# Optimization experiments

Measured on AMD Instinct MI355X. Metric: run time of the kernel, lower is better.

## Reference

```python
import jax, jax.numpy as jnp
import numpy as np

A, B, O, ACT, H, NH = 16, 8192, 128, 16, 128, 4
D = H // NH  # attend_dim
IN = O + ACT
NEG = -1e9


def setup_inputs() -> dict:
    key = jax.random.key(0)
    ks = jax.random.split(key, 16)
    s = lambda k, shape, fan: jax.random.normal(k, shape, jnp.float32) / np.sqrt(fan)
    return {
        "obs": jax.random.normal(ks[0], (A, B, O), jnp.float32),
        "actions": jax.random.uniform(ks[1], (A, B, ACT), jnp.float32),
        # per-agent sa-encoder (enc_fc1)
        "W_sa": s(ks[2], (A, IN, H), IN), "b_sa": jnp.zeros((A, H), jnp.float32),
        # per-agent state encoder (s_enc_fc1)
        "W_s": s(ks[3], (A, O, H), O), "b_s": jnp.zeros((A, H), jnp.float32),
        # shared per-head extractors
        "Wk": s(ks[4], (NH, H, D), H),
        "Wsel": s(ks[5], (NH, H, D), H),
        "Wv": s(ks[6], (NH, H, D), H), "bv": jnp.zeros((NH, D), jnp.float32),
        # per-agent critic MLP
        "Wc1": s(ks[7], (A, 2 * H, H), 2 * H), "bc1": jnp.zeros((A, H), jnp.float32),
        "Wc2": s(ks[8], (A, H, ACT), H), "bc2": jnp.zeros((A, ACT), jnp.float32),
    }


def _bn(x):
    # BatchNorm1d(affine=False) in training mode: normalize over batch axis, biased var
    m = x.mean(axis=1, keepdims=True)
    v = x.var(axis=1, keepdims=True)
    return (x - m) / jnp.sqrt(v + 1e-5)


def reference(obs, actions, W_sa, b_sa, W_s, b_s, Wk, Wsel, Wv, bv, Wc1, bc1, Wc2, bc2):
    lrelu = jax.nn.leaky_relu  # slope 0.01, matches torch default
    inp = jnp.concatenate([obs, actions], axis=-1)            # [A,B,IN]
    sa = lrelu(jnp.einsum('abi,aih->abh', _bn(inp), W_sa) + b_sa[:, None, :])  # [A,B,H]
    se = lrelu(jnp.einsum('abo,aoh->abh', _bn(obs), W_s) + b_s[:, None, :])    # [A,B,H]
    keys = jnp.einsum('abh,nhd->nabd', sa, Wk)                # [NH,A,B,D]
    vals = lrelu(jnp.einsum('abh,nhd->nabd', sa, Wv) + bv[:, None, None, :])
    sel = jnp.einsum('abh,nhd->nabd', se, Wsel)
    logits = jnp.einsum('nibd,njbd->nibj', sel, keys) / np.sqrt(D)  # [NH,A,B,A]
    self_mask = jnp.eye(A, dtype=bool)[None, :, None, :]      # mask j == i
    w = jax.nn.softmax(jnp.where(self_mask, NEG, logits), axis=-1)
    other = jnp.einsum('nibj,njbd->nibd', w, vals)            # [NH,A,B,D]
    other = jnp.transpose(other, (1, 2, 0, 3)).reshape(A, B, NH * D)  # head-order concat
    cin = jnp.concatenate([se, other], axis=-1)               # [A,B,2H]
    h = lrelu(jnp.einsum('abk,akh->abh', cin, Wc1) + bc1[:, None, :])
    all_q = jnp.einsum('abh,aho->abo', h, Wc2) + bc2[:, None, :]      # [A,B,ACT]
    idx = jnp.argmax(actions, axis=-1)[..., None]             # int_acs, [A,B,1]
    q = jnp.take_along_axis(all_q, idx, axis=-1)              # [A,B,1]
    return q
```

## Files before the change

### kernel.cpp

```cpp
#include <hip/hip_runtime.h>
#include <hip/hip_bf16.h>

#define A_N 16
#define B_N 8192
#define O_N 128
#define ACT_N 16
#define H_N 128
#define NH_N 4
#define D_N 32
#define IN_N 144
#define NEGV -1e9f

typedef __attribute__((ext_vector_type(8))) short short8;
typedef __attribute__((ext_vector_type(4))) float floatx4;

static __device__ inline unsigned short f2bf(float f) {
    union { float f; unsigned u; } x{f};
    unsigned u = x.u + 0x7FFFu + ((x.u >> 16) & 1u);
    return (unsigned short)(u >> 16);
}
static __device__ inline unsigned pack_bf2(float a, float b) {
    union { float f; unsigned u; } xa{a}, xb{b};
    unsigned ua = xa.u + 0x7FFFu + ((xa.u >> 16) & 1u);
    unsigned ub = xb.u + 0x7FFFu + ((xb.u >> 16) & 1u);
    return (ua >> 16) | (ub & 0xFFFF0000u);
}
static __device__ inline float bf2f(unsigned short h) {
    union { unsigned u; float f; } x;
    x.u = ((unsigned)h) << 16;
    return x.f;
}
static __device__ inline float bflo(unsigned u) {
    union { unsigned u; float f; } x; x.u = u << 16; return x.f;
}
static __device__ inline float bfhi(unsigned u) {
    union { unsigned u; float f; } x; x.u = u & 0xFFFF0000u; return x.f;
}
static __device__ inline short8 ld_frag(const unsigned* p) {
    union { unsigned u[4]; short8 v; } x;
    uint2 lo = *(const uint2*)p;
    uint2 hi = *(const uint2*)(p + 2);
    x.u[0] = lo.x; x.u[1] = lo.y; x.u[2] = hi.x; x.u[3] = hi.y;
    return x.v;
}

__global__ __launch_bounds__(256) void k_zero(float* p, int n) {
    int i = blockIdx.x * 256 + threadIdx.x;
    if (i < n) p[i] = 0.f;
}

__global__ __launch_bounds__(256) void k_stats(const float* __restrict__ obs,
                                               const float* __restrict__ act,
                                               float* __restrict__ gsum,
                                               float* __restrict__ gsq) {
    __shared__ float ssum[IN_N];
    __shared__ float ssq[IN_N];
    int a = blockIdx.x >> 5;
    int r0 = (blockIdx.x & 31) * 256;
    int t = threadIdx.x;
    if (t < IN_N) { ssum[t] = 0.f; ssq[t] = 0.f; }
    __syncthreads();
    if (t < 128) {
        const float* p = obs + ((size_t)a * B_N + r0) * O_N + t;
        float s = 0.f, q = 0.f;
#pragma unroll 4
        for (int r = 0; r < 256; ++r) {
            float v = p[(size_t)r * O_N];
            s += v; q += v * v;
        }
        ssum[t] = s; ssq[t] = q;
    } else {
        int tt = t - 128;
        int f = tt & 15, rg = tt >> 4;
        const float* p = act + ((size_t)a * B_N + r0 + rg) * ACT_N + f;
        float s = 0.f, q = 0.f;
#pragma unroll 4
        for (int i = 0; i < 32; ++i) {
            float v = p[(size_t)i * 8 * ACT_N];
            s += v; q += v * v;
        }
        atomicAdd(&ssum[O_N + f], s);
        atomicAdd(&ssq[O_N + f], q);
    }
    __syncthreads();
    if (t < IN_N) {
        atomicAdd(&gsum[a * IN_N + t], ssum[t]);
        atomicAdd(&gsq[a * IN_N + t], ssq[t]);
    }
}

__global__ __launch_bounds__(256) void k_finalize(float* gsum, float* gsq) {
    int i = blockIdx.x * 256 + threadIdx.x;
    if (i < A_N * IN_N) {
        const float invB = 1.f / (float)B_N;
        float m = gsum[i] * invB;
        float v = fmaxf(gsq[i] * invB - m * m, 0.f);
        gsum[i] = m;
        gsq[i] = rsqrtf(v + 1e-5f);
    }
}

#define L1E 393216
#define P1E 409600
#define P2E 417792
#define CRE 679936
#define C2E 712704
__global__ __launch_bounds__(256) void k_wprep(
    const float* __restrict__ W_sa, const float* __restrict__ W_s,
    const float* __restrict__ Wk, const float* __restrict__ Wsel,
    const float* __restrict__ Wv, const float* __restrict__ Wc1,
    const float* __restrict__ Wc2, const float* __restrict__ rstd,
    unsigned* __restrict__ wt_l1, unsigned* __restrict__ wt_p1,
    unsigned* __restrict__ wt_p2, unsigned* __restrict__ wt_cr,
    float* __restrict__ wt_c2) {
    int idx = blockIdx.x * 256 + threadIdx.x;
    if (idx < L1E) {
        int a = idx / 24576, rem = idx % 24576;
        int n = rem & 255, kp = rem >> 8;
        int k0 = 2 * kp, k1 = k0 + 1;
        float v0 = 0.f, v1 = 0.f;
        if (n < 128) {
            if (k0 < IN_N) v0 = W_sa[((size_t)a * IN_N + k0) * H_N + n] * rstd[a * IN_N + k0];
            if (k1 < IN_N) v1 = W_sa[((size_t)a * IN_N + k1) * H_N + n] * rstd[a * IN_N + k1];
        } else {
            int m = n - 128;
            if (k0 < O_N) v0 = W_s[((size_t)a * O_N + k0) * H_N + m] * rstd[a * IN_N + k0];
            if (k1 < O_N) v1 = W_s[((size_t)a * O_N + k1) * H_N + m] * rstd[a * IN_N + k1];
        }
        wt_l1[(size_t)a * 24576 + n * 96 + kp] = pack_bf2(v0, v1);
    } else if (idx < P1E) {
        int i2 = idx - L1E;
        int n = i2 & 255, kp = i2 >> 8;
        int k0 = 2 * kp;
        float v0, v1;
        if (n < 128) {
            const float* w = Wk + ((size_t)(n >> 5) * H_N) * D_N + (n & 31);
            v0 = w[(size_t)k0 * D_N]; v1 = w[(size_t)(k0 + 1) * D_N];
        } else {
            int m = n - 128;
            const float* w = Wv + ((size_t)(m >> 5) * H_N) * D_N + (m & 31);
            v0 = w[(size_t)k0 * D_N]; v1 = w[(size_t)(k0 + 1) * D_N];
        }
        wt_p1[n * 64 + kp] = pack_bf2(v0, v1);
    } else if (idx < P2E) {
        int i3 = idx - P1E;
        int n = i3 & 127, kp = i3 >> 7;
        int k0 = 2 * kp;
        const float* w = Wsel + ((size_t)(n >> 5) * H_N) * D_N + (n & 31);
        wt_p2[n * 64 + kp] = pack_bf2(w[(size_t)k0 * D_N], w[(size_t)(k0 + 1) * D_N]);
    } else if (idx < CRE) {
        int i4 = idx - P2E;
        int a = i4 >> 14, r = i4 & 16383;
        int n = r & 127, kp = r >> 7;
        int k0 = 2 * kp;
        const float* w = Wc1 + (size_t)a * 256 * H_N + n;
        wt_cr[(size_t)a * 16384 + n * 128 + kp] =
            pack_bf2(w[(size_t)k0 * H_N], w[(size_t)(k0 + 1) * H_N]);
    } else if (idx < C2E) {
        int i5 = idx - CRE;
        int a = i5 >> 11, rem = i5 & 2047;
        int oo = rem >> 7, h = rem & 127;
        wt_c2[i5] = Wc2[((size_t)a * H_N + h) * ACT_N + oo];
    }
}

__global__ __launch_bounds__(256) void k_bfold(
    const float* __restrict__ mean, const float* __restrict__ rstd,
    const float* __restrict__ W_sa, const float* __restrict__ W_s,
    const float* __restrict__ b_sa, const float* __restrict__ b_s,
    float* __restrict__ fb) {
    int a = blockIdx.x, c = threadIdx.x;
    float s = 0.f;
    if (c < 128) {
        for (int k = 0; k < IN_N; ++k)
            s += mean[a * IN_N + k] * rstd[a * IN_N + k] *
                 W_sa[((size_t)a * IN_N + k) * H_N + c];
        fb[a * 128 + c] = b_sa[a * H_N + c] - s;
    } else {
        int m = c - 128;
        for (int k = 0; k < O_N; ++k)
            s += mean[a * IN_N + k] * rstd[a * IN_N + k] *
                 W_s[((size_t)a * O_N + k) * H_N + m];
        fb[2048 + a * 128 + m] = b_s[a * H_N + m] - s;
    }
}

__global__ __launch_bounds__(256, 3) void k_l1(
    const float* __restrict__ obs, const float* __restrict__ act,
    const unsigned* __restrict__ wt_l1, const float* __restrict__ fb,
    unsigned short* __restrict__ sa_us, unsigned short* __restrict__ se_us,
    int b0g, int Bc) {
    __shared__ unsigned smem[(128 + 128) * 34];
    unsigned* Xs = smem;
    unsigned* Ws = smem + 128 * 34;

    int a = blockIdx.y;
    int z = blockIdx.z;
    int b0 = blockIdx.x * 128;
    int t = threadIdx.x;
    int wid = t >> 6, lane = t & 63, lm = lane & 15, lq = lane >> 4;
    int wrow = (wid & 1) * 64;
    int wcol = (wid >> 1) * 64;

    int kchunks = z ? 2 : 3;
    int kstop = z ? 128 : 160;
    const float* bias = fb + z * 2048 + a * 128;
    unsigned short* outp = z ? se_us : sa_us;

    floatx4 acc[4][4];
#pragma unroll
    for (int mt = 0; mt < 4; ++mt)
#pragma unroll
        for (int nt = 0; nt < 4; ++nt)
#pragma unroll
            for (int e = 0; e < 4; ++e) acc[mt][nt][e] = 0.f;

    const unsigned* WtA = wt_l1 + (size_t)a * 24576 + (size_t)(z * 128) * 96;

    for (int c = 0; c < kchunks; ++c) {
        int kk = c * 64;
        __syncthreads();
        for (int idx = t; idx < 128 * 16; idx += 256) {
            int r = idx >> 4, c4 = idx & 15;
            int k = kk + c4 * 4;
            size_t grow = (size_t)a * B_N + b0g + b0 + r;
            float4 v;
            if (k < O_N) v = *(const float4*)&obs[grow * O_N + k];
            else if (!z && k < IN_N) v = *(const float4*)&act[grow * ACT_N + (k - O_N)];
            else v = make_float4(0.f, 0.f, 0.f, 0.f);
            uint2* dst = (uint2*)&Xs[r * 34 + c4 * 2];
            *dst = make_uint2(pack_bf2(v.x, v.y), pack_bf2(v.z, v.w));
        }
        for (int idx = t; idx < 128 * 8; idx += 256) {
            int n = idx >> 3, c4 = idx & 7;
            uint4 w = *(const uint4*)&WtA[(size_t)n * 96 + (kk >> 1) + c4 * 4];
            uint2* dst = (uint2*)&Ws[n * 34 + c4 * 4];
            dst[0] = make_uint2(w.x, w.y);
            dst[1] = make_uint2(w.z, w.w);
        }
        __syncthreads();
#pragma unroll
        for (int s = 0; s < 2; ++s) {
            if (kk + s * 32 >= kstop) break;
            short8 afr[4];
#pragma unroll
            for (int mt = 0; mt < 4; ++mt)
                afr[mt] = ld_frag(&Xs[(wrow + mt * 16 + lm) * 34 + s * 16 + lq * 4]);
#pragma unroll
            for (int nt = 0; nt < 4; ++nt) {
                short8 bfr = ld_frag(&Ws[(wcol + nt * 16 + lm) * 34 + s * 16 + lq * 4]);
#pragma unroll
                for (int mt = 0; mt < 4; ++mt)
                    acc[mt][nt] = __builtin_amdgcn_mfma_f32_16x16x32_bf16(
                        afr[mt], bfr, acc[mt][nt], 0, 0, 0);
            }
        }
    }

#pragma unroll
    for (int mt = 0; mt < 4; ++mt)
#pragma unroll
        for (int nt = 0; nt < 4; ++nt)
#pragma unroll
            for (int r = 0; r < 4; ++r) {
                int row = b0 + wrow + mt * 16 + lq * 4 + r;
                int col = wcol + nt * 16 + lm;
                float v = acc[mt][nt][r] + bias[col];
                v = v > 0.f ? v : 0.01f * v;
                outp[((size_t)a * Bc + row) * 128 + col] = f2bf(v);
            }
}

__global__ __launch_bounds__(256, 3) void k_fused(
    const unsigned* __restrict__ sa_u, const unsigned* __restrict__ se_u,
    const unsigned* __restrict__ wt_p1, const unsigned* __restrict__ wt_p2,
    const float* __restrict__ bv, unsigned short* __restrict__ other_us,
    int Bc) {
    __shared__ unsigned Xs[64 * 66];
    __shared__ unsigned short keys_s[64 * 130];
    __shared__ unsigned short vals_s[64 * 136];
    unsigned short* sel_s = (unsigned short*)Xs;

    int bg0 = blockIdx.x * 4;
    int t = threadIdx.x;
    int wid = t >> 6, lane = t & 63, lm = lane & 15, lq = lane >> 4;
    int wcol = wid * 32;

    for (int idx = t; idx < 64 * 16; idx += 256) {
        int r = idx >> 4, c4 = idx & 15;
        int a = r >> 2, b = bg0 + (r & 3);
        uint4 v = *(const uint4*)&sa_u[((size_t)a * Bc + b) * 64 + c4 * 4];
        uint2* dst = (uint2*)&Xs[r * 66 + c4 * 4];
        dst[0] = make_uint2(v.x, v.y);
        dst[1] = make_uint2(v.z, v.w);
    }
    uint4 seR[4];
#pragma unroll
    for (int ii = 0; ii < 4; ++ii) {
        int idx = t + ii * 256;
        int r = idx >> 4, c4 = idx & 15;
        int a = r >> 2, b = bg0 + (r & 3);
        seR[ii] = *(const uint4*)&se_u[((size_t)a * Bc + b) * 64 + c4 * 4];
    }
    __syncthreads();

#pragma unroll
    for (int pass = 0; pass < 2; ++pass) {
        floatx4 acc[4][2];
#pragma unroll
        for (int mt = 0; mt < 4; ++mt)
#pragma unroll
            for (int nt = 0; nt < 2; ++nt)
#pragma unroll
                for (int e = 0; e < 4; ++e) acc[mt][nt][e] = 0.f;
        const unsigned* wbase = wt_p1 + (size_t)(pass * 128) * 64;
#pragma unroll
        for (int s = 0; s < 4; ++s) {
            short8 afr[4];
#pragma unroll
            for (int mt = 0; mt < 4; ++mt)
                afr[mt] = ld_frag(&Xs[(mt * 16 + lm) * 66 + s * 16 + lq * 4]);
#pragma unroll
            for (int nt = 0; nt < 2; ++nt) {
                int col = wcol + nt * 16 + lm;
                short8 bfr = ld_frag(wbase + (size_t)col * 64 + s * 16 + lq * 4);
#pragma unroll
                for (int mt = 0; mt < 4; ++mt)
                    acc[mt][nt] = __builtin_amdgcn_mfma_f32_16x16x32_bf16(
                        afr[mt], bfr, acc[mt][nt], 0, 0, 0);
            }
        }
#pragma unroll
        for (int mt = 0; mt < 4; ++mt)
#pragma unroll
            for (int nt = 0; nt < 2; ++nt)
#pragma unroll
                for (int r = 0; r < 4; ++r) {
                    int row = mt * 16 + lq * 4 + r;
                    int col = wcol + nt * 16 + lm;
                    float v = acc[mt][nt][r];
                    if (pass == 0) {
                        keys_s[row * 130 + col] = f2bf(v);
                    } else {
                        v += bv[col];
                        v = v > 0.f ? v : 0.01f * v;
                        vals_s[row * 136 + col] = f2bf(v);
                    }
                }
    }
    __syncthreads();

#pragma unroll
    for (int ii = 0; ii < 4; ++ii) {
        int idx = t + ii * 256;
        int r = idx >> 4, c4 = idx & 15;
        uint2* dst = (uint2*)&Xs[r * 66 + c4 * 4];
        dst[0] = make_uint2(seR[ii].x, seR[ii].y);
        dst[1] = make_uint2(seR[ii].z, seR[ii].w);
    }
    __syncthreads();

    {
        floatx4 acc[4][2];
#pragma unroll
        for (int mt = 0; mt < 4; ++mt)
#pragma unroll
            for (int nt = 0; nt < 2; ++nt)
#pragma unroll
                for (int e = 0; e < 4; ++e) acc[mt][nt][e] = 0.f;
#pragma unroll
        for (int s = 0; s < 4; ++s) {
            short8 afr[4];
#pragma unroll
            for (int mt = 0; mt < 4; ++mt)
                afr[mt] = ld_frag(&Xs[(mt * 16 + lm) * 66 + s * 16 + lq * 4]);
#pragma unroll
            for (int nt = 0; nt < 2; ++nt) {
                int col = wcol + nt * 16 + lm;
                short8 bfr = ld_frag(wt_p2 + (size_t)col * 64 + s * 16 + lq * 4);
#pragma unroll
                for (int mt = 0; mt < 4; ++mt)
                    acc[mt][nt] = __builtin_amdgcn_mfma_f32_16x16x32_bf16(
                        afr[mt], bfr, acc[mt][nt], 0, 0, 0);
            }
        }
        __syncthreads();
#pragma unroll
        for (int mt = 0; mt < 4; ++mt)
#pragma unroll
            for (int nt = 0; nt < 2; ++nt)
#pragma unroll
                for (int r = 0; r < 4; ++r) {
                    int row = mt * 16 + lq * 4 + r;
                    int col = wcol + nt * 16 + lm;
                    sel_s[row * 130 + col] = f2bf(acc[mt][nt][r]);
                }
    }
    __syncthreads();

    const unsigned* keysU = (const unsigned*)keys_s;
    floatx4 lgacc[4];
#pragma unroll
    for (int n = 0; n < 4; ++n) {
        short8 afr = ld_frag(&Xs[(lm * 4 + wid) * 65 + n * 16 + lq * 4]);
        short8 bfr = ld_frag(&keysU[(lm * 4 + wid) * 65 + n * 16 + lq * 4]);
        floatx4 z4 = {0.f, 0.f, 0.f, 0.f};
        lgacc[n] = __builtin_amdgcn_mfma_f32_16x16x32_bf16(afr, bfr, z4, 0, 0, 0);
    }
    __syncthreads();

    float* lgs = (float*)keys_s;
#pragma unroll
    for (int n = 0; n < 4; ++n)
#pragma unroll
        for (int r = 0; r < 4; ++r) {
            int i = lq * 4 + r;
            lgs[((wid * 4 + n) * 16 + i) * 16 + lm] =
                lgacc[n][r] * 0.17677669529663687f;
        }

    int bsub = wid, n = (t >> 4) & 3, i = t & 15;
    float lg[16];
    {
        const float4* lgp = (const float4*)&lgs[((bsub * 4 + n) * 16 + i) * 16];
#pragma unroll
        for (int c = 0; c < 4; ++c) {
            float4 v = lgp[c];
            lg[4 * c] = v.x; lg[4 * c + 1] = v.y;
            lg[4 * c + 2] = v.z; lg[4 * c + 3] = v.w;
        }
    }
    lg[i] = NEGV;
    float m = lg[0];
#pragma unroll
    for (int j = 1; j < 16; ++j) m = fmaxf(m, lg[j]);
    float sum = 0.f;
#pragma unroll
    for (int j = 0; j < 16; ++j) { lg[j] = __expf(lg[j] - m); sum += lg[j]; }
    float inv = 1.f / sum;
#pragma unroll
    for (int j = 0; j < 16; ++j) lg[j] *= inv;

    const unsigned* valsU = (const unsigned*)vals_s;
    float ov[32];
#pragma unroll
    for (int u = 0; u < 32; ++u) ov[u] = 0.f;
#pragma unroll
    for (int j = 0; j < 16; ++j) {
        const uint4* vrow = (const uint4*)&valsU[(j * 4 + bsub) * 68 + n * 16];
        float w = lg[j];
#pragma unroll
        for (int c = 0; c < 4; ++c) {
            uint4 x = vrow[c];
            ov[8 * c + 0] = fmaf(w, bflo(x.x), ov[8 * c + 0]);
            ov[8 * c + 1] = fmaf(w, bfhi(x.x), ov[8 * c + 1]);
            ov[8 * c + 2] = fmaf(w, bflo(x.y), ov[8 * c + 2]);
            ov[8 * c + 3] = fmaf(w, bfhi(x.y), ov[8 * c + 3]);
            ov[8 * c + 4] = fmaf(w, bflo(x.z), ov[8 * c + 4]);
            ov[8 * c + 5] = fmaf(w, bfhi(x.z), ov[8 * c + 5]);
            ov[8 * c + 6] = fmaf(w, bflo(x.w), ov[8 * c + 6]);
            ov[8 * c + 7] = fmaf(w, bfhi(x.w), ov[8 * c + 7]);
        }
    }
    {
        uint4* orow = (uint4*)&other_us[((size_t)i * Bc + bg0 + bsub) * 128 + n * 32];
#pragma unroll
        for (int h = 0; h < 2; ++h) {
            uint4 o;
            o.x = pack_bf2(ov[16 * h + 0], ov[16 * h + 1]);
            o.y = pack_bf2(ov[16 * h + 2], ov[16 * h + 3]);
            o.z = pack_bf2(ov[16 * h + 4], ov[16 * h + 5]);
            o.w = pack_bf2(ov[16 * h + 6], ov[16 * h + 7]);
            orow[2 * h] = o;
            o.x = pack_bf2(ov[16 * h + 8], ov[16 * h + 9]);
            o.y = pack_bf2(ov[16 * h + 10], ov[16 * h + 11]);
            o.z = pack_bf2(ov[16 * h + 12], ov[16 * h + 13]);
            o.w = pack_bf2(ov[16 * h + 14], ov[16 * h + 15]);
            orow[2 * h + 1] = o;
        }
    }
}

__global__ __launch_bounds__(256, 3) void k_critic(
    const unsigned* __restrict__ se_u, const unsigned* __restrict__ other_u,
    const unsigned* __restrict__ wt_cr,
    const float* __restrict__ bc1, const float* __restrict__ actions,
    const float* __restrict__ wt_c2, const float* __restrict__ bc2,
    float* __restrict__ qout, int b0g, int Bc) {
    __shared__ unsigned smem[(64 + 128) * 34];
    unsigned* Xs = smem;
    unsigned* Ws = smem + 64 * 34;

    int a = blockIdx.y;
    int b0 = blockIdx.x * 64;
    int t = threadIdx.x;
    int wid = t >> 6, lane = t & 63, lm = lane & 15, lq = lane >> 4;
    int wrow = (wid & 1) * 32;
    int wcol = (wid >> 1) * 64;

    floatx4 acc[2][4];
#pragma unroll
    for (int mt = 0; mt < 2; ++mt)
#pragma unroll
        for (int nt = 0; nt < 4; ++nt)
#pragma unroll
            for (int e = 0; e < 4; ++e) acc[mt][nt][e] = 0.f;

    const unsigned* WtA = wt_cr + (size_t)a * 16384;

    for (int c = 0; c < 4; ++c) {
        int kk = c * 64;
        __syncthreads();
        const unsigned* src = (c < 2) ? se_u : other_u;
        int off = (c & 1) * 32;
        for (int idx = t; idx < 64 * 8; idx += 256) {
            int r = idx >> 3, c4 = idx & 7;
            uint4 v = *(const uint4*)&src[((size_t)a * Bc + b0 + r) * 64 + off + c4 * 4];
            uint2* dst = (uint2*)&Xs[r * 34 + c4 * 4];
            dst[0] = make_uint2(v.x, v.y);
            dst[1] = make_uint2(v.z, v.w);
        }
        for (int idx = t; idx < 128 * 8; idx += 256) {
            int n = idx >> 3, c4 = idx & 7;
            uint4 w = *(const uint4*)&WtA[(size_t)n * 128 + (kk >> 1) + c4 * 4];
            uint2* dst = (uint2*)&Ws[n * 34 + c4 * 4];
            dst[0] = make_uint2(w.x, w.y);
            dst[1] = make_uint2(w.z, w.w);
        }
        __syncthreads();
#pragma unroll
        for (int s = 0; s < 2; ++s) {
            short8 afr[2];
#pragma unroll
            for (int mt = 0; mt < 2; ++mt)
                afr[mt] = ld_frag(&Xs[(wrow + mt * 16 + lm) * 34 + s * 16 + lq * 4]);
#pragma unroll
            for (int nt = 0; nt < 4; ++nt) {
                short8 bfr = ld_frag(&Ws[(wcol + nt * 16 + lm) * 34 + s * 16 + lq * 4]);
#pragma unroll
                for (int mt = 0; mt < 2; ++mt)
                    acc[mt][nt] = __builtin_amdgcn_mfma_f32_16x16x32_bf16(
                        afr[mt], bfr, acc[mt][nt], 0, 0, 0);
            }
        }
    }

    __syncthreads();
    unsigned short* hbuf = (unsigned short*)smem;
#pragma unroll
    for (int mt = 0; mt < 2; ++mt)
#pragma unroll
        for (int nt = 0; nt < 4; ++nt)
#pragma unroll
            for (int r = 0; r < 4; ++r) {
                int row = wrow + mt * 16 + lq * 4 + r;
                int col = wcol + nt * 16 + lm;
                float v = acc[mt][nt][r] + bc1[a * H_N + col];
                v = v > 0.f ? v : 0.01f * v;
                hbuf[row * 132 + col] = f2bf(v);
            }
    __syncthreads();
    if (t < 64) {
        size_t arow = (size_t)a * B_N + b0g + b0 + t;
        const float* ap = &actions[arow * ACT_N];
        float bestv = ap[0];
        int bi = 0;
        for (int o = 1; o < ACT_N; ++o) {
            float v = ap[o];
            if (v > bestv) { bestv = v; bi = o; }
        }
        float q = bc2[a * ACT_N + bi];
        const float4* w4p = (const float4*)&wt_c2[((size_t)a * ACT_N + bi) * H_N];
        const uint2* hp2 = (const uint2*)&hbuf[t * 132];
#pragma unroll
        for (int h4 = 0; h4 < 32; ++h4) {
            float4 w4 = w4p[h4];
            uint2 hh = hp2[h4];
            q = fmaf(bflo(hh.x), w4.x, q);
            q = fmaf(bfhi(hh.x), w4.y, q);
            q = fmaf(bflo(hh.y), w4.z, q);
            q = fmaf(bfhi(hh.y), w4.w, q);
        }
        qout[arow] = q;
    }
}

extern "C" void kernel_launch(void* const* d_in, const int* in_sizes, int n_in,
                              void* d_out, int out_size, void* d_ws, size_t ws_size,
                              hipStream_t stream) {
    const float* obs     = (const float*)d_in[0];
    const float* actions = (const float*)d_in[1];
    const float* W_sa    = (const float*)d_in[2];
    const float* b_sa    = (const float*)d_in[3];
    const float* W_s     = (const float*)d_in[4];
    const float* b_s     = (const float*)d_in[5];
    const float* Wk      = (const float*)d_in[6];
    const float* Wsel    = (const float*)d_in[7];
    const float* Wv      = (const float*)d_in[8];
    const float* bv      = (const float*)d_in[9];
    const float* Wc1     = (const float*)d_in[10];
    const float* bc1     = (const float*)d_in[11];
    const float* Wc2     = (const float*)d_in[12];
    const float* bc2     = (const float*)d_in[13];
    float* out = (float*)d_out;
    char* ws = (char*)d_ws;

    size_t o = 0;
    float* gsum = (float*)(ws + o); o += 2304 * 4;
    float* gsq  = (float*)(ws + o); o += 2304 * 4;
    unsigned* wt_l1 = (unsigned*)(ws + o); o += (size_t)393216 * 4;
    unsigned* wt_p1 = (unsigned*)(ws + o); o += (size_t)16384 * 4;
    unsigned* wt_p2 = (unsigned*)(ws + o); o += (size_t)8192 * 4;
    unsigned* wt_cr = (unsigned*)(ws + o); o += (size_t)262144 * 4;
    float* fb = (float*)(ws + o); o += (size_t)4096 * 4;
    float* wt_c2 = (float*)(ws + o); o += (size_t)32768 * 4;
    size_t fixed = o;

    int Bc = B_N;
    while (Bc > 128 && fixed + 12288ull * Bc > ws_size) Bc >>= 1;

    unsigned short* sa_us = (unsigned short*)(ws + o); o += (size_t)A_N * Bc * 128 * 2;
    unsigned short* se_us = (unsigned short*)(ws + o); o += (size_t)A_N * Bc * 128 * 2;
    unsigned short* ot_us = (unsigned short*)(ws + o); o += (size_t)A_N * Bc * 128 * 2;

    k_zero<<<dim3(18), 256, 0, stream>>>(gsum, 2 * A_N * IN_N);
    k_stats<<<dim3(A_N * 32), 256, 0, stream>>>(obs, actions, gsum, gsq);
    k_finalize<<<dim3(9), 256, 0, stream>>>(gsum, gsq);
    k_wprep<<<dim3(C2E / 256), 256, 0, stream>>>(W_sa, W_s, Wk, Wsel, Wv, Wc1, Wc2,
                                                 gsq, wt_l1, wt_p1, wt_p2, wt_cr, wt_c2);
    k_bfold<<<dim3(A_N), 256, 0, stream>>>(gsum, gsq, W_sa, W_s, b_sa, b_s, fb);

    for (int b0g = 0; b0g < B_N; b0g += Bc) {
        k_l1<<<dim3(Bc / 128, A_N, 2), 256, 0, stream>>>(
            obs, actions, wt_l1, fb, sa_us, se_us, b0g, Bc);
        k_fused<<<dim3(Bc / 4), 256, 0, stream>>>(
            (const unsigned*)sa_us, (const unsigned*)se_us, wt_p1, wt_p2, bv,
            ot_us, Bc);
        k_critic<<<dim3(Bc / 64, A_N), 256, 0, stream>>>(
            (const unsigned*)se_us, (const unsigned*)ot_us, wt_cr, bc1,
            actions, wt_c2, bc2, out, b0g, Bc);
    }
}
```

Before: 324.9 us.

## Merge sa/se encoder blocks and switch intermediates to batch-major agent-interleaved layout

k_l1 now computes both the sa and se encoders in one 512-thread block, so each obs tile is loaded and converted to bf16 once instead of twice. The sa/se/other intermediates are stored as [B][A][H] instead of [A][B][H], which makes k_fused's per-batch-group gather a contiguous read and changes k_critic to a strided per-agent read. LDS strides and row orderings in k_fused are adjusted to match the new layout, and k_critic's occupancy hint is raised. The se half of the merged block still runs the padded actions chunk through the zero-weight rows, and the critic reads are less coalesced.

```diff
diff --git a/kernel.cpp b/kernel.cpp
--- a/kernel.cpp
+++ b/kernel.cpp
@@ -185,28 +185,22 @@
     }
 }
 
-__global__ __launch_bounds__(256, 3) void k_l1(
+__global__ __launch_bounds__(512, 2) void k_l1(
     const float* __restrict__ obs, const float* __restrict__ act,
     const unsigned* __restrict__ wt_l1, const float* __restrict__ fb,
     unsigned short* __restrict__ sa_us, unsigned short* __restrict__ se_us,
     int b0g, int Bc) {
-    __shared__ unsigned smem[(128 + 128) * 34];
+    __shared__ unsigned smem[(128 + 256) * 34];
     unsigned* Xs = smem;
     unsigned* Ws = smem + 128 * 34;
 
     int a = blockIdx.y;
-    int z = blockIdx.z;
     int b0 = blockIdx.x * 128;
     int t = threadIdx.x;
     int wid = t >> 6, lane = t & 63, lm = lane & 15, lq = lane >> 4;
     int wrow = (wid & 1) * 64;
     int wcol = (wid >> 1) * 64;
 
-    int kchunks = z ? 2 : 3;
-    int kstop = z ? 128 : 160;
-    const float* bias = fb + z * 2048 + a * 128;
-    unsigned short* outp = z ? se_us : sa_us;
-
     floatx4 acc[4][4];
 #pragma unroll
     for (int mt = 0; mt < 4; ++mt)
@@ -215,23 +209,23 @@
 #pragma unroll
             for (int e = 0; e < 4; ++e) acc[mt][nt][e] = 0.f;
 
-    const unsigned* WtA = wt_l1 + (size_t)a * 24576 + (size_t)(z * 128) * 96;
-
-    for (int c = 0; c < kchunks; ++c) {
+    const unsigned* WtA = wt_l1 + (size_t)a * 24576;
+
+    for (int c = 0; c < 3; ++c) {
         int kk = c * 64;
         __syncthreads();
-        for (int idx = t; idx < 128 * 16; idx += 256) {
+        for (int idx = t; idx < 128 * 16; idx += 512) {
             int r = idx >> 4, c4 = idx & 15;
             int k = kk + c4 * 4;
             size_t grow = (size_t)a * B_N + b0g + b0 + r;
             float4 v;
             if (k < O_N) v = *(const float4*)&obs[grow * O_N + k];
-            else if (!z && k < IN_N) v = *(const float4*)&act[grow * ACT_N + (k - O_N)];
+            else if (k < IN_N) v = *(const float4*)&act[grow * ACT_N + (k - O_N)];
             else v = make_float4(0.f, 0.f, 0.f, 0.f);
             uint2* dst = (uint2*)&Xs[r * 34 + c4 * 2];
             *dst = make_uint2(pack_bf2(v.x, v.y), pack_bf2(v.z, v.w));
         }
-        for (int idx = t; idx < 128 * 8; idx += 256) {
+        for (int idx = t; idx < 256 * 8; idx += 512) {
             int n = idx >> 3, c4 = idx & 7;
             uint4 w = *(const uint4*)&WtA[(size_t)n * 96 + (kk >> 1) + c4 * 4];
             uint2* dst = (uint2*)&Ws[n * 34 + c4 * 4];
@@ -241,7 +235,7 @@
         __syncthreads();
 #pragma unroll
         for (int s = 0; s < 2; ++s) {
-            if (kk + s * 32 >= kstop) break;
+            if (kk + s * 32 >= 160) break;
             short8 afr[4];
 #pragma unroll
             for (int mt = 0; mt < 4; ++mt)
@@ -257,17 +251,21 @@
         }
     }
 
+    int zsel = (wcol >= 128);
+    unsigned short* outp = zsel ? se_us : sa_us;
+    const float* bias = fb + zsel * 2048 + a * 128;
+    int cbase = wcol & 127;
 #pragma unroll
     for (int mt = 0; mt < 4; ++mt)
 #pragma unroll
         for (int nt = 0; nt < 4; ++nt)
 #pragma unroll
             for (int r = 0; r < 4; ++r) {
-                int row = b0 + wrow + mt * 16 + lq * 4 + r;
-                int col = wcol + nt * 16 + lm;
+                int row = wrow + mt * 16 + lq * 4 + r;
+                int col = cbase + nt * 16 + lm;
                 float v = acc[mt][nt][r] + bias[col];
                 v = v > 0.f ? v : 0.01f * v;
-                outp[((size_t)a * Bc + row) * 128 + col] = f2bf(v);
+                outp[((size_t)(b0 + row) * 16 + a) * 128 + col] = f2bf(v);
             }
 }
 
@@ -286,10 +284,12 @@
     int wid = t >> 6, lane = t & 63, lm = lane & 15, lq = lane >> 4;
     int wcol = wid * 32;
 
+    const unsigned* sa_base = sa_u + (size_t)(bg0 * 16) * 64;
+    const unsigned* se_base = se_u + (size_t)(bg0 * 16) * 64;
+
     for (int idx = t; idx < 64 * 16; idx += 256) {
         int r = idx >> 4, c4 = idx & 15;
-        int a = r >> 2, b = bg0 + (r & 3);
-        uint4 v = *(const uint4*)&sa_u[((size_t)a * Bc + b) * 64 + c4 * 4];
+        uint4 v = *(const uint4*)&sa_base[(size_t)idx * 4];
         uint2* dst = (uint2*)&Xs[r * 66 + c4 * 4];
         dst[0] = make_uint2(v.x, v.y);
         dst[1] = make_uint2(v.z, v.w);
@@ -298,9 +298,7 @@
 #pragma unroll
     for (int ii = 0; ii < 4; ++ii) {
         int idx = t + ii * 256;
-        int r = idx >> 4, c4 = idx & 15;
-        int a = r >> 2, b = bg0 + (r & 3);
-        seR[ii] = *(const uint4*)&se_u[((size_t)a * Bc + b) * 64 + c4 * 4];
+        seR[ii] = *(const uint4*)&se_base[(size_t)idx * 4];
     }
     __syncthreads();
 
@@ -393,7 +391,7 @@
                 for (int r = 0; r < 4; ++r) {
                     int row = mt * 16 + lq * 4 + r;
                     int col = wcol + nt * 16 + lm;
-                    sel_s[row * 130 + col] = f2bf(acc[mt][nt][r]);
+                    sel_s[row * 132 + col] = f2bf(acc[mt][nt][r]);
                 }
     }
     __syncthreads();
@@ -402,8 +400,8 @@
     floatx4 lgacc[4];
 #pragma unroll
     for (int n = 0; n < 4; ++n) {
-        short8 afr = ld_frag(&Xs[(lm * 4 + wid) * 65 + n * 16 + lq * 4]);
-        short8 bfr = ld_frag(&keysU[(lm * 4 + wid) * 65 + n * 16 + lq * 4]);
+        short8 afr = ld_frag(&Xs[(wid * 16 + lm) * 66 + n * 16 + lq * 4]);
+        short8 bfr = ld_frag(&keysU[(wid * 16 + lm) * 65 + n * 16 + lq * 4]);
         floatx4 z4 = {0.f, 0.f, 0.f, 0.f};
         lgacc[n] = __builtin_amdgcn_mfma_f32_16x16x32_bf16(afr, bfr, z4, 0, 0, 0);
     }
@@ -447,7 +445,7 @@
     for (int u = 0; u < 32; ++u) ov[u] = 0.f;
 #pragma unroll
     for (int j = 0; j < 16; ++j) {
-        const uint4* vrow = (const uint4*)&valsU[(j * 4 + bsub) * 68 + n * 16];
+        const uint4* vrow = (const uint4*)&valsU[(bsub * 16 + j) * 68 + n * 16];
         float w = lg[j];
 #pragma unroll
         for (int c = 0; c < 4; ++c) {
@@ -463,7 +461,7 @@
         }
     }
     {
-        uint4* orow = (uint4*)&other_us[((size_t)i * Bc + bg0 + bsub) * 128 + n * 32];
+        uint4* orow = (uint4*)&other_us[((size_t)(bg0 + bsub) * 16 + i) * 128 + n * 32];
 #pragma unroll
         for (int h = 0; h < 2; ++h) {
             uint4 o;
@@ -481,7 +479,7 @@
     }
 }
 
-__global__ __launch_bounds__(256, 3) void k_critic(
+__global__ __launch_bounds__(256, 4) void k_critic(
     const unsigned* __restrict__ se_u, const unsigned* __restrict__ other_u,
     const unsigned* __restrict__ wt_cr,
     const float* __restrict__ bc1, const float* __restrict__ actions,
@@ -515,7 +513,7 @@
         int off = (c & 1) * 32;
         for (int idx = t; idx < 64 * 8; idx += 256) {
             int r = idx >> 3, c4 = idx & 7;
-            uint4 v = *(const uint4*)&src[((size_t)a * Bc + b0 + r) * 64 + off + c4 * 4];
+            uint4 v = *(const uint4*)&src[((size_t)(b0 + r) * 16 + a) * 64 + off + c4 * 4];
             uint2* dst = (uint2*)&Xs[r * 34 + c4 * 4];
             dst[0] = make_uint2(v.x, v.y);
             dst[1] = make_uint2(v.z, v.w);
@@ -631,7 +629,7 @@
     k_bfold<<<dim3(A_N), 256, 0, stream>>>(gsum, gsq, W_sa, W_s, b_sa, b_s, fb);
 
     for (int b0g = 0; b0g < B_N; b0g += Bc) {
-        k_l1<<<dim3(Bc / 128, A_N, 2), 256, 0, stream>>>(
+        k_l1<<<dim3(Bc / 128, A_N), 512, 0, stream>>>(
             obs, actions, wt_l1, fb, sa_us, se_us, b0g, Bc);
         k_fused<<<dim3(Bc / 4), 256, 0, stream>>>(
             (const unsigned*)sa_us, (const unsigned*)se_us, wt_p1, wt_p2, bv,
```

New measurement: 317.7 us. 2.2% less time.
